# Kernel optimization log

Measured on AMD Instinct MI355X. Metric: run time of the kernel, lower is better.

Reference implementation:

```python
import jax, jax.numpy as jnp
import numpy as np

NUM_NODES = 100_000
NUM_EDGES = 3_200_000
THETA = 1.0  # module hyperparameter (default 1.0)


def setup_inputs() -> dict:
    key = jax.random.key(0)
    k_v, k_src, k_dst, k_t1, k_t2, k_r = jax.random.split(key, 6)
    v = jax.random.normal(k_v, (NUM_NODES,), dtype=jnp.float32)
    src = jax.random.randint(k_src, (NUM_EDGES,), 0, NUM_NODES, dtype=jnp.int32)
    dst = jax.random.randint(k_dst, (NUM_EDGES,), 0, NUM_NODES, dtype=jnp.int32)
    theta_sd_1 = jax.random.normal(k_t1, (NUM_EDGES,), dtype=jnp.float32) * 0.1
    theta_sd_2 = jax.random.normal(k_t2, (NUM_EDGES,), dtype=jnp.float32) * 0.1
    # conductance = 1/resistance, resistance in (0.5, 2.0) -> conductance in (0.5, 2.0)
    conductance = 1.0 / jax.random.uniform(k_r, (NUM_EDGES,), dtype=jnp.float32, minval=0.5, maxval=2.0)
    return {"t": 0, "v": v, "src": src, "dst": dst,
            "theta_sd_1": theta_sd_1, "theta_sd_2": theta_sd_2,
            "conductance": conductance}


def reference(t, v, src, dst, theta_sd_1, theta_sd_2, conductance):
    # per-edge gated current: g(vs, vd) = relu(theta1*(vs - vd) + theta2)
    diff = v[src] - v[dst]                                   # [E]
    current = conductance * jax.nn.relu(theta_sd_1 * diff + theta_sd_2)  # [E]
    incoming = jax.ops.segment_sum(current, dst, num_segments=NUM_NODES)  # [N]
    outgoing = jax.ops.segment_sum(current, src, num_segments=NUM_NODES)  # [N]
    return (incoming - outgoing) / THETA
```

## Files before the change

### kernel.cpp

```cpp
#include <hip/hip_runtime.h>
#include <hip/hip_fp16.h>


#define RL      14
#define RANGE   (1 << RL)
#define NB      8
#define P0_BLK  256
#define P0_EPT  4
#define P0_EPB  (P0_BLK * P0_EPT)
#define SCAP    512
#define P1_BLK  1024
#define NSLICE  32

__global__ __launch_bounds__(P0_BLK) void p0_kernel(
    const float* __restrict__ v,
    const int*   __restrict__ src,
    const int*   __restrict__ dst,
    const float* __restrict__ t1,
    const float* __restrict__ t2,
    const float* __restrict__ cond,
    unsigned*    __restrict__ entries,
    int*         __restrict__ cursors,
    int E, int EC)
{
    __shared__ unsigned sbuf[NB][SCAP];
    __shared__ int scnt[NB], gbase[NB];

    if (threadIdx.x < NB) scnt[threadIdx.x] = 0;
    __syncthreads();

    const int i0 = blockIdx.x * P0_EPB + (int)threadIdx.x * P0_EPT;

    #define EMIT(node, mag, signbit)                                         \
        {                                                                    \
            int rr = (node) >> RL;                                           \
            unsigned en = (((unsigned)((node) & (RANGE - 1))) << 17) |       \
                          ((unsigned)(signbit) << 16) |                      \
                          (unsigned)__half_as_ushort(__float2half(mag));     \
            int idx = atomicAdd(&scnt[rr], 1);                               \
            if (idx < SCAP) sbuf[rr][idx] = en;                              \
        }

    if (i0 + P0_EPT <= E) {
        int4   s4 = *(const int4*)  (src  + i0);
        int4   d4 = *(const int4*)  (dst  + i0);
        float4 a4 = *(const float4*)(t1   + i0);
        float4 b4 = *(const float4*)(t2   + i0);
        float4 c4 = *(const float4*)(cond + i0);

        float vs0 = v[s4.x], vs1 = v[s4.y], vs2 = v[s4.z], vs3 = v[s4.w];
        float vd0 = v[d4.x], vd1 = v[d4.y], vd2 = v[d4.z], vd3 = v[d4.w];

        float x0 = fmaf(a4.x, vs0 - vd0, b4.x);
        float x1 = fmaf(a4.y, vs1 - vd1, b4.y);
        float x2 = fmaf(a4.z, vs2 - vd2, b4.z);
        float x3 = fmaf(a4.w, vs3 - vd3, b4.w);

        if (x0 > 0.0f) { float c = c4.x * x0; EMIT(d4.x, c, 0u) EMIT(s4.x, c, 1u) }
        if (x1 > 0.0f) { float c = c4.y * x1; EMIT(d4.y, c, 0u) EMIT(s4.y, c, 1u) }
        if (x2 > 0.0f) { float c = c4.z * x2; EMIT(d4.z, c, 0u) EMIT(s4.z, c, 1u) }
        if (x3 > 0.0f) { float c = c4.w * x3; EMIT(d4.w, c, 0u) EMIT(s4.w, c, 1u) }
    } else {
        for (int i = i0; i < E && i < i0 + P0_EPT; ++i) {
            int s = src[i], d = dst[i];
            float x = fmaf(t1[i], v[s] - v[d], t2[i]);
            if (x > 0.0f) { float c = cond[i] * x; EMIT(d, c, 0u) EMIT(s, c, 1u) }
        }
    }
    #undef EMIT

    __syncthreads();
    if (threadIdx.x < NB) {
        int c = min(scnt[threadIdx.x], SCAP);
        gbase[threadIdx.x] = atomicAdd(&cursors[threadIdx.x], c);
    }
    __syncthreads();

    for (int r = 0; r < NB; ++r) {
        const int c  = min(scnt[r], SCAP);
        const int gb = gbase[r];
        unsigned* g = entries + (size_t)r * EC;
        for (int j = threadIdx.x; j < c; j += P0_BLK)
            if (gb + j < EC) g[gb + j] = sbuf[r][j];
    }
}

__global__ __launch_bounds__(P1_BLK) void p1_kernel(
    const unsigned* __restrict__ entries,
    const int*      __restrict__ cursors,
    float*          __restrict__ partial,
    int N, int EC)
{
    __shared__ __align__(16) float acc[RANGE];

    const int r    = blockIdx.x / NSLICE;
    const int s    = blockIdx.x % NSLICE;
    const int base = r << RL;
    const int len  = min(RANGE, N - base);

    for (int i = threadIdx.x; i < RANGE; i += P1_BLK) acc[i] = 0.0f;
    __syncthreads();

    const int cnt = min(cursors[r], EC);
    const int seg = (cnt + NSLICE - 1) / NSLICE;
    const int e0  = s * seg;
    const int e1  = min(cnt, e0 + seg);
    const unsigned* p = entries + (size_t)r * EC;

    for (int j = e0 + (int)threadIdx.x; j < e1; j += P1_BLK) {
        unsigned e = p[j];
        float mag = __half2float(__ushort_as_half((unsigned short)(e & 0xFFFFu)));
        atomicAdd(&acc[e >> 17], (e & 0x10000u) ? -mag : mag);
    }

    __syncthreads();
    float* op = partial + (size_t)s * N + base;
    const int len4 = (len > 0) ? (len & ~3) : 0;
    for (int i = (int)threadIdx.x * 4; i < len4; i += P1_BLK * 4)
        *(float4*)(op + i) = *(const float4*)&acc[i];
    for (int i = len4 + (int)threadIdx.x; i < len; i += P1_BLK)
        op[i] = acc[i];
}

__global__ __launch_bounds__(256) void reduce_kernel(
    const float* __restrict__ partial, float* __restrict__ out, int N4)
{
    int n = blockIdx.x * blockDim.x + threadIdx.x;
    if (n < N4) {
        float4 sm = make_float4(0.f, 0.f, 0.f, 0.f);
        for (int p = 0; p < NSLICE; ++p) {
            float4 q = ((const float4*)partial)[(size_t)p * N4 + n];
            sm.x += q.x; sm.y += q.y; sm.z += q.z; sm.w += q.w;
        }
        ((float4*)out)[n] = sm;
    }
}

__global__ __launch_bounds__(256) void reduce_scalar_kernel(
    const float* __restrict__ partial, float* __restrict__ out, int N)
{
    int n = blockIdx.x * blockDim.x + threadIdx.x;
    if (n < N) {
        float sm = 0.0f;
        for (int p = 0; p < NSLICE; ++p) sm += partial[(size_t)p * N + n];
        out[n] = sm;
    }
}

__global__ __launch_bounds__(256) void atomic_fallback_kernel(
    const float* __restrict__ v, const int* __restrict__ src, const int* __restrict__ dst,
    const float* __restrict__ t1, const float* __restrict__ t2, const float* __restrict__ cond,
    float* __restrict__ out, int E)
{
    int i = blockIdx.x * blockDim.x + threadIdx.x;
    int stride = gridDim.x * blockDim.x;
    for (; i < E; i += stride) {
        int s = src[i], d = dst[i];
        float x = fmaf(t1[i], v[s] - v[d], t2[i]);
        if (x > 0.0f) {
            float c = cond[i] * x;
            atomicAdd(&out[d], c);
            atomicAdd(&out[s], -c);
        }
    }
}

extern "C" void kernel_launch(void* const* d_in, const int* in_sizes, int n_in,
                              void* d_out, int out_size, void* d_ws, size_t ws_size,
                              hipStream_t stream) {
    const float* v    = (const float*)d_in[1];
    const int*   src  = (const int*)  d_in[2];
    const int*   dst  = (const int*)  d_in[3];
    const float* t1   = (const float*)d_in[4];
    const float* t2   = (const float*)d_in[5];
    const float* cond = (const float*)d_in[6];
    float* out = (float*)d_out;
    const int E = in_sizes[2];
    const int N = out_size;

    const int EC = (int)((((size_t)E * 2 * RANGE) / (size_t)(N > 0 ? N : 1)
                          + (size_t)E / 8 + 4096) & ~(size_t)255);

    const size_t entBytes = (size_t)NB * EC * sizeof(unsigned);
    const size_t curBytes = 256;
    const size_t parBytes = (size_t)NSLICE * N * sizeof(float);

    const bool ok = (N <= NB * RANGE) &&
                    (entBytes + curBytes + parBytes <= ws_size);

    if (ok) {
        unsigned* entries = (unsigned*)d_ws;
        int*      cursors = (int*)((char*)d_ws + entBytes);
        float*    partial = (float*)((char*)d_ws + entBytes + curBytes);

        hipMemsetAsync(cursors, 0, curBytes, stream);

        const int G = (E + P0_EPB - 1) / P0_EPB;
        p0_kernel<<<G, P0_BLK, 0, stream>>>(v, src, dst, t1, t2, cond,
                                            entries, cursors, E, EC);

        const int R = (N + RANGE - 1) / RANGE;
        p1_kernel<<<R * NSLICE, P1_BLK, 0, stream>>>(entries, cursors, partial, N, EC);

        if ((N & 3) == 0) {
            const int N4 = N / 4;
            reduce_kernel<<<(N4 + 255) / 256, 256, 0, stream>>>(partial, out, N4);
        } else {
            reduce_scalar_kernel<<<(N + 255) / 256, 256, 0, stream>>>(partial, out, N);
        }
    } else {
        hipMemsetAsync(out, 0, (size_t)N * sizeof(float), stream);
        int grid = (E + 255) / 256;
        if (grid > 2048) grid = 2048;
        atomic_fallback_kernel<<<grid, 256, 0, stream>>>(v, src, dst, t1, t2, cond, out, E);
    }
}
```

Baseline: 87.24 us.

## Replace global atomic cursors with per-block fixed-slot bins and counts

The edge phase now writes each block's per-range entries into a fixed slot of SCAP entries indexed by block and range, plus a count array, instead of reserving space through global atomic cursors. This removes the cursor memset and the contention on global atomics. The accumulate phase assigns one wave per block bin and reads the counts into shared memory first. Edge-stream loads become nontemporal. In exchange, each wave reads a short bin with partial lanes idle, and the workspace grows to NB*G*SCAP entries.

```diff
diff --git a/kernel.cpp b/kernel.cpp
--- a/kernel.cpp
+++ b/kernel.cpp
@@ -11,6 +11,10 @@
 #define SCAP    512
 #define P1_BLK  1024
 #define NSLICE  32
+#define MAXSEG  128
+
+typedef int   vi4 __attribute__((ext_vector_type(4)));
+typedef float vf4 __attribute__((ext_vector_type(4)));
 
 __global__ __launch_bounds__(P0_BLK) void p0_kernel(
     const float* __restrict__ v,
@@ -19,17 +23,18 @@
     const float* __restrict__ t1,
     const float* __restrict__ t2,
     const float* __restrict__ cond,
-    unsigned*    __restrict__ entries,
-    int*         __restrict__ cursors,
-    int E, int EC)
+    unsigned*    __restrict__ bins,
+    int*         __restrict__ counts,
+    int E, int G)
 {
     __shared__ unsigned sbuf[NB][SCAP];
-    __shared__ int scnt[NB], gbase[NB];
+    __shared__ int scnt[NB];
 
     if (threadIdx.x < NB) scnt[threadIdx.x] = 0;
     __syncthreads();
 
-    const int i0 = blockIdx.x * P0_EPB + (int)threadIdx.x * P0_EPT;
+    const int blk = blockIdx.x;
+    const int i0  = blk * P0_EPB + (int)threadIdx.x * P0_EPT;
 
     #define EMIT(node, mag, signbit)                                         \
         {                                                                    \
@@ -42,11 +47,11 @@
         }
 
     if (i0 + P0_EPT <= E) {
-        int4   s4 = *(const int4*)  (src  + i0);
-        int4   d4 = *(const int4*)  (dst  + i0);
-        float4 a4 = *(const float4*)(t1   + i0);
-        float4 b4 = *(const float4*)(t2   + i0);
-        float4 c4 = *(const float4*)(cond + i0);
+        vi4 s4 = __builtin_nontemporal_load((const vi4*)(src  + i0));
+        vi4 d4 = __builtin_nontemporal_load((const vi4*)(dst  + i0));
+        vf4 a4 = __builtin_nontemporal_load((const vf4*)(t1   + i0));
+        vf4 b4 = __builtin_nontemporal_load((const vf4*)(t2   + i0));
+        vf4 c4 = __builtin_nontemporal_load((const vf4*)(cond + i0));
 
         float vs0 = v[s4.x], vs1 = v[s4.y], vs2 = v[s4.z], vs3 = v[s4.w];
         float vd0 = v[d4.x], vd1 = v[d4.y], vd2 = v[d4.z], vd3 = v[d4.w];
@@ -70,56 +75,61 @@
     #undef EMIT
 
     __syncthreads();
-    if (threadIdx.x < NB) {
-        int c = min(scnt[threadIdx.x], SCAP);
-        gbase[threadIdx.x] = atomicAdd(&cursors[threadIdx.x], c);
-    }
-    __syncthreads();
+    if (threadIdx.x < NB)
+        counts[threadIdx.x * G + blk] = min(scnt[threadIdx.x], SCAP);
 
     for (int r = 0; r < NB; ++r) {
-        const int c  = min(scnt[r], SCAP);
-        const int gb = gbase[r];
-        unsigned* g = entries + (size_t)r * EC;
-        for (int j = threadIdx.x; j < c; j += P0_BLK)
-            if (gb + j < EC) g[gb + j] = sbuf[r][j];
+        const int c = min(scnt[r], SCAP);
+        unsigned* g = bins + ((size_t)r * G + blk) * SCAP;
+        for (int j = threadIdx.x; j < c; j += P0_BLK) g[j] = sbuf[r][j];
     }
 }
 
 __global__ __launch_bounds__(P1_BLK) void p1_kernel(
-    const unsigned* __restrict__ entries,
-    const int*      __restrict__ cursors,
+    const unsigned* __restrict__ bins,
+    const int*      __restrict__ counts,
     float*          __restrict__ partial,
-    int N, int EC)
+    int N, int G)
 {
     __shared__ __align__(16) float acc[RANGE];
+    __shared__ int gcnt[MAXSEG];
 
     const int r    = blockIdx.x / NSLICE;
     const int s    = blockIdx.x % NSLICE;
     const int base = r << RL;
     const int len  = min(RANGE, N - base);
 
+    const int seg = (G + NSLICE - 1) / NSLICE;
+    const int g0  = s * seg;
+    const int g1  = min(G, g0 + seg);
+    const int ng  = g1 - g0;
+
     for (int i = threadIdx.x; i < RANGE; i += P1_BLK) acc[i] = 0.0f;
-    __syncthreads();
-
-    const int cnt = min(cursors[r], EC);
-    const int seg = (cnt + NSLICE - 1) / NSLICE;
-    const int e0  = s * seg;
-    const int e1  = min(cnt, e0 + seg);
-    const unsigned* p = entries + (size_t)r * EC;
-
-    for (int j = e0 + (int)threadIdx.x; j < e1; j += P1_BLK) {
-        unsigned e = p[j];
-        float mag = __half2float(__ushort_as_half((unsigned short)(e & 0xFFFFu)));
-        atomicAdd(&acc[e >> 17], (e & 0x10000u) ? -mag : mag);
-    }
-
-    __syncthreads();
-    float* op = partial + (size_t)s * N + base;
-    const int len4 = (len > 0) ? (len & ~3) : 0;
-    for (int i = (int)threadIdx.x * 4; i < len4; i += P1_BLK * 4)
-        *(float4*)(op + i) = *(const float4*)&acc[i];
-    for (int i = len4 + (int)threadIdx.x; i < len; i += P1_BLK)
-        op[i] = acc[i];
+    for (int i = threadIdx.x; i < ng; i += P1_BLK) gcnt[i] = counts[r * G + g0 + i];
+    __syncthreads();
+
+    const int wave = threadIdx.x >> 6;
+    const int lane = threadIdx.x & 63;
+
+    for (int gi = wave; gi < ng; gi += (P1_BLK / 64)) {
+        const int c = gcnt[gi];
+        const unsigned* p = bins + ((size_t)r * G + g0 + gi) * SCAP;
+        for (int j = lane; j < c; j += 64) {
+            unsigned e = p[j];
+            float mag = __half2float(__ushort_as_half((unsigned short)(e & 0xFFFFu)));
+            atomicAdd(&acc[e >> 17], (e & 0x10000u) ? -mag : mag);
+        }
+    }
+
+    __syncthreads();
+    if (len > 0) {
+        float* op = partial + (size_t)s * N + base;
+        const int len4 = len & ~3;
+        for (int i = (int)threadIdx.x * 4; i < len4; i += P1_BLK * 4)
+            *(float4*)(op + i) = *(const float4*)&acc[i];
+        for (int i = len4 + (int)threadIdx.x; i < len; i += P1_BLK)
+            op[i] = acc[i];
+    }
 }
 
 __global__ __launch_bounds__(256) void reduce_kernel(
@@ -178,29 +188,26 @@
     const int E = in_sizes[2];
     const int N = out_size;
 
-    const int EC = (int)((((size_t)E * 2 * RANGE) / (size_t)(N > 0 ? N : 1)
-                          + (size_t)E / 8 + 4096) & ~(size_t)255);
-
-    const size_t entBytes = (size_t)NB * EC * sizeof(unsigned);
-    const size_t curBytes = 256;
+    const int G = (E + P0_EPB - 1) / P0_EPB;
+
+    const size_t binBytes = (size_t)NB * G * SCAP * sizeof(unsigned);
+    const size_t cntBytes = (((size_t)NB * G * 4) + 255) & ~(size_t)255;
     const size_t parBytes = (size_t)NSLICE * N * sizeof(float);
 
-    const bool ok = (N <= NB * RANGE) &&
-                    (entBytes + curBytes + parBytes <= ws_size);
+    const bool ok = (N <= NB * RANGE) && (E > 0) &&
+                    ((G + NSLICE - 1) / NSLICE <= MAXSEG) &&
+                    (binBytes + cntBytes + parBytes <= ws_size);
 
     if (ok) {
-        unsigned* entries = (unsigned*)d_ws;
-        int*      cursors = (int*)((char*)d_ws + entBytes);
-        float*    partial = (float*)((char*)d_ws + entBytes + curBytes);
-
-        hipMemsetAsync(cursors, 0, curBytes, stream);
-
-        const int G = (E + P0_EPB - 1) / P0_EPB;
+        unsigned* bins    = (unsigned*)d_ws;
+        int*      counts  = (int*)((char*)d_ws + binBytes);
+        float*    partial = (float*)((char*)d_ws + binBytes + cntBytes);
+
         p0_kernel<<<G, P0_BLK, 0, stream>>>(v, src, dst, t1, t2, cond,
-                                            entries, cursors, E, EC);
+                                            bins, counts, E, G);
 
         const int R = (N + RANGE - 1) / RANGE;
-        p1_kernel<<<R * NSLICE, P1_BLK, 0, stream>>>(entries, cursors, partial, N, EC);
+        p1_kernel<<<R * NSLICE, P1_BLK, 0, stream>>>(bins, counts, partial, N, G);
 
         if ((N & 3) == 0) {
             const int N4 = N / 4;
@@ -209,7 +216,7 @@
             reduce_scalar_kernel<<<(N + 255) / 256, 256, 0, stream>>>(partial, out, N);
         }
     } else {
-        hipMemsetAsync(out, 0, (size_t)N * sizeof(float), stream);
+        (void)hipMemsetAsync(out, 0, (size_t)N * sizeof(float), stream);
         int grid = (E + 255) / 256;
         if (grid > 2048) grid = 2048;
         atomic_fallback_kernel<<<grid, 256, 0, stream>>>(v, src, dst, t1, t2, cond, out, E);
```

Result: faster. 76.22 us (-12.6%).
